# Optimization experiments

Measured on AMD Instinct MI355X. Metric: run time of the kernel, lower is better.

## Reference

```python
import math
import jax, jax.numpy as jnp
import numpy as np

HIDDEN = 1024
NUM_HEADS = 16
HEAD_DIM = HIDDEN // NUM_HEADS
B, S = 4, 2048


def setup_inputs() -> dict:
    key = jax.random.key(0)
    ks = jax.random.split(key, 10)
    sc_in = 1.0 / math.sqrt(HIDDEN)
    inp = {
        "query": jax.random.normal(ks[0], (B, S, HIDDEN), jnp.float32),
        "key": jax.random.normal(ks[1], (B, S, HIDDEN), jnp.float32),
        "value": jax.random.normal(ks[2], (B, S, HIDDEN), jnp.float32),
        "mask": jax.random.randint(ks[3], (B, S), 0, 2).astype(bool),
        # NOTE: ModuleList([Linear]*num_heads) shares ONE Linear across all heads.
        "Wq": jax.random.normal(ks[4], (HIDDEN, HEAD_DIM), jnp.float32) * sc_in,
        "bq": jnp.zeros((HEAD_DIM,), jnp.float32),
        "Wk": jax.random.normal(ks[5], (HIDDEN, HEAD_DIM), jnp.float32) * sc_in,
        "bk": jnp.zeros((HEAD_DIM,), jnp.float32),
        "Wv": jax.random.normal(ks[6], (HIDDEN, HEAD_DIM), jnp.float32) * sc_in,
        "bv": jnp.zeros((HEAD_DIM,), jnp.float32),
        "Wout": jax.random.normal(ks[7], (HIDDEN, HIDDEN), jnp.float32) * sc_in,
        "bout": jnp.zeros((HIDDEN,), jnp.float32),
        "seq_mask": 0,
    }
    return inp


def _layer_norm_scores(x, eps=1e-8):
    # torch.std is unbiased (ddof=1); is_train=False => no affine
    mean = jnp.mean(x, axis=-1, keepdims=True)
    sigma = jnp.std(x, axis=-1, keepdims=True, ddof=1)
    return (x - mean) / (sigma + eps)


def reference(query, key, value, mask, Wq, bq, Wk, bk, Wv, bv, Wout, bout, seq_mask):
    # All heads share identical weights -> compute one head, tile the concat.
    q = query @ Wq + bq          # [B,S,hd]
    k = key @ Wk + bk            # [B,S,hd]
    v = value @ Wv + bv          # [B,S,hd]
    scores = jnp.einsum("bqd,bkd->bqk", q, k) / math.sqrt(HIDDEN)  # [B,S,S]
    scores = _layer_norm_scores(scores)
    m = jnp.broadcast_to(mask[:, None, :], scores.shape)  # [B,S,S]
    if seq_mask:
        tri = jnp.triu(jnp.ones(scores.shape[-2:], bool), k=1)
        m = m | tri[None]
    # original fills with -1e-32 (effectively a no-op bug) -- reproduce exactly
    scores = scores + jnp.where(m, jnp.float32(-1e-32), jnp.float32(0.0))
    attn = jax.nn.softmax(scores, axis=-1)
    head = jnp.einsum("bqk,bkd->bqd", attn, v)   # [B,S,hd]
    attention = jnp.tile(head, (1, 1, NUM_HEADS))  # concat of identical heads
    return attention @ Wout + bout
```

## Files before the change

### kernel.cpp

```cpp
#include <hip/hip_runtime.h>
#include <math.h>

#define B_  4
#define S_  2048
#define H_  1024
#define D_  64
#define ROWS (B_*S_)
#define KSPLIT 8
#define LOG2E 1.4426950408889634f

typedef __attribute__((ext_vector_type(4))) float  floatx4;
typedef __attribute__((ext_vector_type(8))) short  short8;
typedef __attribute__((ext_vector_type(8))) __bf16 bf16x8;

#define WS_KSUM 0
#define WS_M    (WS_KSUM + B_*D_)
#define WS_A2   (WS_M + B_*D_*D_)
#define WS_C2   (WS_A2 + ROWS)
#define WS_SWP  (WS_C2 + ROWS)
#define WS_FEND (WS_SWP + KSPLIT*ROWS)
#define WB_QB  0
#define WB_KF  (WB_QB + ROWS*D_)
#define WB_VF  (WB_KF + ROWS*D_)
#define WB_WT  (WB_VF + ROWS*D_)
#define WB_WFF (WB_WT + 3*D_*H_)
#define WB_OP  (WB_WFF + H_*D_)
#define NZ2    (B_*D_ + B_*D_*D_)

__device__ __forceinline__ unsigned short f2bf(float f) {
    union { float f; unsigned u; } v; v.f = f;
    unsigned r = v.u + 0x7FFFu + ((v.u >> 16) & 1u);
    return (unsigned short)(r >> 16);
}
__device__ __forceinline__ short bfc(float f) {
    __bf16 h = (__bf16)f;
    short s; __builtin_memcpy(&s, &h, 2); return s;
}
__device__ __forceinline__ float bf2f(short s) {
    union { unsigned u; float f; } v;
    v.u = ((unsigned)(unsigned short)s) << 16; return v.f;
}
__device__ __forceinline__ bf16x8 ldb(const short* p) {
    union { short8 s; bf16x8 b; } u; u.s = *(const short8*)p; return u.b;
}
#define MFMA(a,b,c) __builtin_amdgcn_mfma_f32_16x16x32_bf16(a, b, c, 0, 0, 0)
__device__ __forceinline__ void lds_fence() {
    __builtin_amdgcn_wave_barrier();
    __builtin_amdgcn_s_waitcnt(0xc07f);
    __builtin_amdgcn_wave_barrier();
}

__global__ __launch_bounds__(256) void prep(
    const float* __restrict__ Wq, const float* __restrict__ Wk,
    const float* __restrict__ Wv, const float* __restrict__ Wout,
    float* __restrict__ wsf)
{
    __shared__ float tile[64][65];
    short* wsb = (short*)(wsf + WS_FEND);
    const int bx = blockIdx.x, t = threadIdx.x;
    if (bx < 96) {
        int idx = bx * 256 + t;
        int mat = idx >> 13, rem = idx & 8191;
        int kc = rem >> 8, nt = (rem >> 6) & 3, lane = rem & 63;
        int g = lane >> 4, l15 = lane & 15;
        const float* W = (mat == 0) ? Wq : (mat == 1) ? Wk : Wv;
        short8 fr;
        #pragma unroll
        for (int j = 0; j < 8; ++j)
            fr[j] = (short)f2bf(W[(size_t)(kc*32 + g*8 + j) * D_ + nt*16 + l15]);
        *(short8*)&wsb[WB_WT + (size_t)idx * 8] = fr;
    } else if (bx < 112) {
        int n0 = (bx - 96) * 64;
        int nn = t & 63, dg = t >> 6;
        for (int dd = 0; dd < 16; ++dd) {
            int d = dg * 16 + dd;
            float s = 0.0f;
            #pragma unroll
            for (int h = 0; h < 16; ++h)
                s += Wout[(size_t)(h * 64 + d) * H_ + n0 + nn];
            tile[d][nn] = s;
        }
        __syncthreads();
        #pragma unroll
        for (int u = 0; u < 2; ++u) {
            int s = 2*t + u;
            int ctl = s >> 7, h = (s >> 6) & 1, lane = s & 63;
            int g = lane >> 4, l2 = lane & 15;
            short8 fr;
            #pragma unroll
            for (int j = 0; j < 8; ++j)
                fr[j] = (short)f2bf(tile[h*32 + g*8 + j][ctl*16 + l2]);
            *(short8*)&wsb[WB_WFF + (size_t)((((n0 >> 4) + ctl)*2 + h)*64 + lane) * 8] = fr;
        }
    } else {
        int i = (bx - 112) * 256 + t;
        if (i < NZ2) wsf[WS_KSUM + i] = 0.0f;
    }
}

__global__ __launch_bounds__(256) void qkv_mfma(
    const float* __restrict__ query, const float* __restrict__ key,
    const float* __restrict__ value,
    const float* __restrict__ bq, const float* __restrict__ bk,
    const float* __restrict__ bvp, float* __restrict__ wsf)
{
    short* wsb = (short*)(wsf + WS_FEND);
    const int mat = blockIdx.y;
    const float* X    = (mat == 0) ? query : (mat == 1) ? key : value;
    const float* bias = (mat == 0) ? bq    : (mat == 1) ? bk  : bvp;
    const short* WT3 = wsb + WB_WT + (size_t)mat * (D_ * H_);

    const int t = threadIdx.x, w = t >> 6, lane = t & 63;
    const int l15 = lane & 15, g = lane >> 4;
    const int r0 = blockIdx.x * 32;
    const int mrow0 = (w >> 1) * 16;
    const int nt0 = (w & 1) * 2;

    __shared__ short xs[32][136];
    floatx4 acc[2] = {};

    for (int step = 0; step < 8; ++step) {
        __syncthreads();
        #pragma unroll
        for (int u = 0; u < 4; ++u) {
            int row = u * 8 + (t >> 5), col = (t & 31) * 4;
            float4 xv = *(const float4*)&X[(size_t)(r0 + row) * H_ + step * 128 + col];
            short4 pk;
            pk.x = bfc(xv.x); pk.y = bfc(xv.y); pk.z = bfc(xv.z); pk.w = bfc(xv.w);
            *(short4*)&xs[row][col] = pk;
        }
        __syncthreads();
        #pragma unroll
        for (int kk = 0; kk < 4; ++kk) {
            bf16x8 a = ldb(&xs[mrow0 + l15][kk * 32 + g * 8]);
            int kc = step * 4 + kk;
            #pragma unroll
            for (int n = 0; n < 2; ++n) {
                bf16x8 bf = ldb(&WT3[(size_t)((kc * 4) + nt0 + n) * 512 + lane * 8]);
                acc[n] = MFMA(a, bf, acc[n]);
            }
        }
    }

    if (mat == 0) {
        short* QB = wsb + WB_QB;
        #pragma unroll
        for (int n = 0; n < 2; ++n) {
            int col = (nt0 + n) * 16 + l15;
            float bb = bias[col];
            #pragma unroll
            for (int r = 0; r < 4; ++r)
                QB[(size_t)(r0 + mrow0 + 4*g + r) * D_ + col] = (short)f2bf(acc[n][r] + bb);
        }
    } else if (mat == 1) {
        short* KF = wsb + WB_KF;
        #pragma unroll
        for (int n = 0; n < 2; ++n) {
            int d = (nt0 + n) * 16 + l15;
            int kh = d >> 5, gk = (d >> 3) & 3, j = d & 7;
            float bb = bias[d];
            #pragma unroll
            for (int r = 0; r < 4; ++r) {
                int R = r0 + mrow0 + 4*g + r;
                KF[(size_t)(((R >> 4) * 2 + kh) * 64 + gk * 16 + (R & 15)) * 8 + j] =
                    (short)f2bf(acc[n][r] + bb);
            }
        }
    } else {
        short* VF = wsb + WB_VF;
        int R0 = r0 + mrow0 + 4*g;
        int kh = (R0 >> 5) & 1, gv = (R0 >> 3) & 3, j0 = R0 & 7, blk = R0 >> 6;
        #pragma unroll
        for (int n = 0; n < 2; ++n) {
            int d = (nt0 + n) * 16 + l15;
            int ntv = d >> 4;
            float bb = bias[d];
            short4 pk;
            pk.x = (short)f2bf(acc[n][0] + bb); pk.y = (short)f2bf(acc[n][1] + bb);
            pk.z = (short)f2bf(acc[n][2] + bb); pk.w = (short)f2bf(acc[n][3] + bb);
            *(short4*)&VF[(size_t)(((blk * 4 + ntv) * 2 + kh) * 64 + gv * 16 + (d & 15)) * 8 + j0] = pk;
        }
    }
}

__global__ __launch_bounds__(256) void kstats(float* __restrict__ wsf) {
    const short* KF = (short*)(wsf + WS_FEND) + WB_KF;
    const int b     = blockIdx.x >> 5;
    const int chunk = blockIdx.x & 31;
    const int keyblk0 = b * 128 + chunk * 4;

    __shared__ float kt[64][64];
    const int t = threadIdx.x;
    #pragma unroll
    for (int u = 0; u < 2; ++u) {
        int s = 2*t + u;
        int kb4 = s >> 7, kh = (s >> 6) & 1, lane2 = s & 63;
        int g2 = lane2 >> 4, l2 = lane2 & 15;
        short8 v = *(const short8*)&KF[(size_t)(((keyblk0 + kb4) * 2 + kh) * 64 + lane2) * 8];
        #pragma unroll
        for (int j = 0; j < 8; ++j)
            kt[kb4 * 16 + l2][kh * 32 + g2 * 8 + j] = bf2f(v[j]);
    }
    __syncthreads();

    const int td = t >> 4, te = t & 15;
    float acc[4][4] = {};
    for (int j = 0; j < 64; ++j) {
        float4 a  = *(const float4*)&kt[j][td*4];
        float4 bb = *(const float4*)&kt[j][te*4];
        float av[4] = {a.x, a.y, a.z, a.w};
        float bw[4] = {bb.x, bb.y, bb.z, bb.w};
        #pragma unroll
        for (int i = 0; i < 4; ++i)
            #pragma unroll
            for (int l = 0; l < 4; ++l)
                acc[i][l] += av[i] * bw[l];
    }
    float* M = wsf + WS_M + (size_t)b * D_ * D_;
    #pragma unroll
    for (int i = 0; i < 4; ++i)
        #pragma unroll
        for (int l = 0; l < 4; ++l)
            atomicAdd(&M[(td*4 + i) * D_ + te*4 + l], acc[i][l]);

    if (t < 64) {
        float s = 0.0f;
        for (int j = 0; j < 64; ++j) s += kt[j][t];
        atomicAdd(&wsf[WS_KSUM + b * D_ + t], s);
    }
}

__global__ __launch_bounds__(256) void rowstats(float* __restrict__ wsf) {
    const short* Qb = (short*)(wsf + WS_FEND) + WB_QB;
    const int t = threadIdx.x, w = t >> 6, lane = t & 63;
    const int q0 = blockIdx.x * 32 + w * 8;
    const int b  = q0 >> 11;
    const float* M = wsf + WS_M + (size_t)b * D_ * D_;

    float qv[8], y[8] = {};
    #pragma unroll
    for (int r = 0; r < 8; ++r) qv[r] = bf2f(Qb[(size_t)(q0 + r) * D_ + lane]);
    for (int d2 = 0; d2 < 64; ++d2) {
        float m = M[d2 * D_ + lane];
        #pragma unroll
        for (int r = 0; r < 8; ++r) y[r] += __shfl(qv[r], d2, 64) * m;
    }
    float kl = wsf[WS_KSUM + b * D_ + lane];
    float z[8], sv[8];
    #pragma unroll
    for (int r = 0; r < 8; ++r) { z[r] = y[r] * qv[r]; sv[r] = qv[r] * kl; }
    #pragma unroll
    for (int m = 1; m < 64; m <<= 1) {
        #pragma unroll
        for (int r = 0; r < 8; ++r) {
            z[r]  += __shfl_xor(z[r],  m, 64);
            sv[r] += __shfl_xor(sv[r], m, 64);
        }
    }
    #pragma unroll
    for (int r = 0; r < 8; ++r) {
        if (lane == r) {
            float sum   = sv[r] * (1.0f / 32.0f);
            float sumsq = z[r]  * (1.0f / 1024.0f);
            float mu  = sum * (1.0f / 2048.0f);
            float var = (sumsq - sum * sum * (1.0f / 2048.0f)) * (1.0f / 2047.0f);
            var = fmaxf(var, 0.0f);
            float inv = 1.0f / (sqrtf(var) + 1e-8f);
            wsf[WS_A2 + q0 + r] = inv * (LOG2E / 32.0f);
            wsf[WS_C2 + q0 + r] = -mu * inv * LOG2E;
        }
    }
}

__global__ __launch_bounds__(256) void attention(float* __restrict__ wsf) {
    short* wsb = (short*)(wsf + WS_FEND);
    const short* Qb = wsb + WB_QB;
    const short* KF = wsb + WB_KF;
    const short* VF = wsb + WB_VF;
    __shared__ short P[4][32][72];
    __shared__ short stage[2][8192];

    const int t = threadIdx.x, w = t >> 6, lane = t & 63;
    const int l15 = lane & 15, g = lane >> 4;
    const int q0 = blockIdx.x * 128 + w * 32;
    const int b  = blockIdx.x >> 4;
    const int kb = blockIdx.y * (S_ / KSPLIT);

    bf16x8 bqf[2][2];
    float a2v[2], c2v[2];
    #pragma unroll
    for (int nt = 0; nt < 2; ++nt) {
        int q = q0 + nt*16 + l15;
        #pragma unroll
        for (int h = 0; h < 2; ++h)
            bqf[nt][h] = ldb(&Qb[(size_t)q * D_ + h*32 + g*8]);
        a2v[nt] = wsf[WS_A2 + q];
        c2v[nt] = wsf[WS_C2 + q];
    }

    floatx4 O[2][4] = {};
    float sacc[2] = {0.0f, 0.0f};
    short* Pw = &P[w][0][0];

    const int tb = t * 8;
    short8 rr[4];
    {
        const short* KFc = KF + (size_t)((b * S_ + kb) >> 4) * 1024;
        const short* VFc = VF + (size_t)((b * S_ + kb) >> 6) * 4096;
        rr[0] = *(const short8*)&KFc[tb];
        rr[1] = *(const short8*)&KFc[tb + 2048];
        rr[2] = *(const short8*)&VFc[tb];
        rr[3] = *(const short8*)&VFc[tb + 2048];
    }

    for (int kc = 0; kc < S_ / KSPLIT; kc += 64) {
        short* buf = &stage[(kc >> 6) & 1][0];
        __syncthreads();
        *(short8*)&buf[tb]        = rr[0];
        *(short8*)&buf[tb + 2048] = rr[1];
        *(short8*)&buf[tb + 4096] = rr[2];
        *(short8*)&buf[tb + 6144] = rr[3];
        if (kc + 64 < S_ / KSPLIT) {
            const int key1 = kb + kc + 64;
            const short* KFc = KF + (size_t)((b * S_ + key1) >> 4) * 1024;
            const short* VFc = VF + (size_t)((b * S_ + key1) >> 6) * 4096;
            rr[0] = *(const short8*)&KFc[tb];
            rr[1] = *(const short8*)&KFc[tb + 2048];
            rr[2] = *(const short8*)&VFc[tb];
            rr[3] = *(const short8*)&VFc[tb + 2048];
        }
        __syncthreads();

        floatx4 Sc[4][2] = {};
        #pragma unroll
        for (int kt = 0; kt < 4; ++kt) {
            bf16x8 ak0 = ldb(&buf[(kt*2 + 0)*512 + lane*8]);
            bf16x8 ak1 = ldb(&buf[(kt*2 + 1)*512 + lane*8]);
            #pragma unroll
            for (int nt = 0; nt < 2; ++nt) {
                Sc[kt][nt] = MFMA(ak0, bqf[nt][0], Sc[kt][nt]);
                Sc[kt][nt] = MFMA(ak1, bqf[nt][1], Sc[kt][nt]);
            }
        }
        lds_fence();
        #pragma unroll
        for (int nt = 0; nt < 2; ++nt) {
            const float aa = a2v[nt], cc = c2v[nt];
            #pragma unroll
            for (int kt = 0; kt < 4; ++kt) {
                float w0 = exp2f(fmaf(Sc[kt][nt][0], aa, cc));
                float w1 = exp2f(fmaf(Sc[kt][nt][1], aa, cc));
                float w2 = exp2f(fmaf(Sc[kt][nt][2], aa, cc));
                float w3 = exp2f(fmaf(Sc[kt][nt][3], aa, cc));
                sacc[nt] += (w0 + w1) + (w2 + w3);
                short4 pk;
                pk.x = bfc(w0); pk.y = bfc(w1); pk.z = bfc(w2); pk.w = bfc(w3);
                *(short4*)&Pw[(nt*16 + l15) * 72 + kt*16 + 4*g] = pk;
            }
        }
        lds_fence();
        bf16x8 ap[2][2];
        #pragma unroll
        for (int mt = 0; mt < 2; ++mt)
            #pragma unroll
            for (int kh = 0; kh < 2; ++kh)
                ap[mt][kh] = ldb(&Pw[(mt*16 + l15) * 72 + kh*32 + g*8]);
        #pragma unroll
        for (int nt = 0; nt < 4; ++nt) {
            #pragma unroll
            for (int kh = 0; kh < 2; ++kh) {
                bf16x8 bv = ldb(&buf[4096 + (nt*2 + kh)*512 + lane*8]);
                #pragma unroll
                for (int mt = 0; mt < 2; ++mt)
                    O[mt][nt] = MFMA(ap[mt][kh], bv, O[mt][nt]);
            }
        }
    }

    #pragma unroll
    for (int nt = 0; nt < 2; ++nt) {
        sacc[nt] += __shfl_xor(sacc[nt], 16, 64);
        sacc[nt] += __shfl_xor(sacc[nt], 32, 64);
    }
    if (lane < 16) {
        wsf[WS_SWP + blockIdx.y * ROWS + q0 + lane]      = sacc[0];
        wsf[WS_SWP + blockIdx.y * ROWS + q0 + 16 + lane] = sacc[1];
    }
    short* OP = wsb + WB_OP + ((size_t)blockIdx.y * ROWS + q0) * D_;
    #pragma unroll
    for (int mt = 0; mt < 2; ++mt)
        #pragma unroll
        for (int nt = 0; nt < 4; ++nt)
            #pragma unroll
            for (int r = 0; r < 4; ++r)
                OP[(size_t)(mt*16 + 4*g + r) * D_ + nt*16 + l15] =
                    (short)f2bf(O[mt][nt][r]);
}

__global__ __launch_bounds__(256) void outmm(
    const float* __restrict__ bout, const float* __restrict__ wsf,
    float* __restrict__ out)
{
    const short* wsb = (const short*)(wsf + WS_FEND);
    const short* OP  = wsb + WB_OP;
    const short* WFF = wsb + WB_WFF;
    __shared__ short hnF[2 * 64 * 8];

    const int t = threadIdx.x;
    const int row0 = blockIdx.x * 16;

    {
        const int r = t >> 4;
        const int c = (t & 15) * 4;
        const int row = row0 + r;
        float sw = 0.0f;
        #pragma unroll
        for (int p = 0; p < KSPLIT; ++p) sw += wsf[WS_SWP + p * ROWS + row];
        float inv = 1.0f / sw;
        float a0 = 0.f, a1 = 0.f, a2 = 0.f, a3 = 0.f;
        #pragma unroll
        for (int p = 0; p < KSPLIT; ++p) {
            short4 o = *(const short4*)&OP[((size_t)p * ROWS + row) * D_ + c];
            a0 += bf2f(o.x); a1 += bf2f(o.y); a2 += bf2f(o.z); a3 += bf2f(o.w);
        }
        short4 hn;
        hn.x = (short)f2bf(a0 * inv); hn.y = (short)f2bf(a1 * inv);
        hn.z = (short)f2bf(a2 * inv); hn.w = (short)f2bf(a3 * inv);
        int kh = c >> 5, gH = (c >> 3) & 3, j0 = c & 7;
        *(short4*)&hnF[(size_t)(kh * 64 + gH * 16 + r) * 8 + j0] = hn;
    }
    __syncthreads();

    const int w = t >> 6, lane = t & 63, l15 = lane & 15, g = lane >> 4;
    bf16x8 ah0 = ldb(&hnF[(size_t)(0 * 64 + lane) * 8]);
    bf16x8 ah1 = ldb(&hnF[(size_t)(1 * 64 + lane) * 8]);
    #pragma unroll
    for (int i = 0; i < 16; ++i) {
        int n16 = w * 16 + i;
        floatx4 acc = {};
        acc = MFMA(ah0, ldb(&WFF[(size_t)(n16 * 2 + 0) * 512 + lane * 8]), acc);
        acc = MFMA(ah1, ldb(&WFF[(size_t)(n16 * 2 + 1) * 512 + lane * 8]), acc);
        int col = n16 * 16 + l15;
        float bb = bout[col];
        #pragma unroll
        for (int r = 0; r < 4; ++r)
            out[(size_t)(row0 + 4*g + r) * H_ + col] = acc[r] + bb;
    }
}

extern "C" void kernel_launch(void* const* d_in, const int* in_sizes, int n_in,
                              void* d_out, int out_size, void* d_ws, size_t ws_size,
                              hipStream_t stream) {
    const float* query = (const float*)d_in[0];
    const float* key   = (const float*)d_in[1];
    const float* value = (const float*)d_in[2];
    const float* Wq   = (const float*)d_in[4];
    const float* bq   = (const float*)d_in[5];
    const float* Wk   = (const float*)d_in[6];
    const float* bk   = (const float*)d_in[7];
    const float* Wv   = (const float*)d_in[8];
    const float* bv   = (const float*)d_in[9];
    const float* Wout = (const float*)d_in[10];
    const float* bout = (const float*)d_in[11];

    float* ws  = (float*)d_ws;
    float* out = (float*)d_out;

    prep<<<177, 256, 0, stream>>>(Wq, Wk, Wv, Wout, ws);
    qkv_mfma<<<dim3(ROWS/32, 3), 256, 0, stream>>>(query, key, value, bq, bk, bv, ws);
    kstats<<<B_ * 32, 256, 0, stream>>>(ws);
    rowstats<<<ROWS/32, 256, 0, stream>>>(ws);
    attention<<<dim3(ROWS/128, KSPLIT), 256, 0, stream>>>(ws);
    outmm<<<ROWS/16, 256, 0, stream>>>(bout, ws, out);
}
```

Measured before the change: 202.1 us.

## Load K/V fragments directly from global in attention, halve block size, double key split

Removes the double-buffered LDS staging of K and V tiles in the attention kernel. Each wave now loads MFMA fragments straight from global memory. Blocks shrink to two waves with a launch-bounds occupancy hint, and the key dimension is split sixteen ways instead of eight to keep the grid large. It also adds s_setprio around the MFMA sections and uses the hardware exp2 intrinsic. In exchange it loses K/V reuse across waves through LDS, raising L2 traffic, and the final reduction over key splits gets more partials.

```diff
diff --git a/kernel.cpp b/kernel.cpp
--- a/kernel.cpp
+++ b/kernel.cpp
@@ -6,7 +6,7 @@
 #define H_  1024
 #define D_  64
 #define ROWS (B_*S_)
-#define KSPLIT 8
+#define KSPLIT 16
 #define LOG2E 1.4426950408889634f
 
 typedef __attribute__((ext_vector_type(4))) float  floatx4;
@@ -272,18 +272,17 @@
     }
 }
 
-__global__ __launch_bounds__(256) void attention(float* __restrict__ wsf) {
+__global__ __launch_bounds__(128, 3) void attention(float* __restrict__ wsf) {
     short* wsb = (short*)(wsf + WS_FEND);
     const short* Qb = wsb + WB_QB;
     const short* KF = wsb + WB_KF;
     const short* VF = wsb + WB_VF;
-    __shared__ short P[4][32][72];
-    __shared__ short stage[2][8192];
+    __shared__ short P[2][32][72];
 
     const int t = threadIdx.x, w = t >> 6, lane = t & 63;
     const int l15 = lane & 15, g = lane >> 4;
-    const int q0 = blockIdx.x * 128 + w * 32;
-    const int b  = blockIdx.x >> 4;
+    const int q0 = blockIdx.x * 64 + w * 32;
+    const int b  = blockIdx.x >> 5;
     const int kb = blockIdx.y * (S_ / KSPLIT);
 
     bf16x8 bqf[2][2];
@@ -302,56 +301,33 @@
     float sacc[2] = {0.0f, 0.0f};
     short* Pw = &P[w][0][0];
 
-    const int tb = t * 8;
-    short8 rr[4];
-    {
-        const short* KFc = KF + (size_t)((b * S_ + kb) >> 4) * 1024;
-        const short* VFc = VF + (size_t)((b * S_ + kb) >> 6) * 4096;
-        rr[0] = *(const short8*)&KFc[tb];
-        rr[1] = *(const short8*)&KFc[tb + 2048];
-        rr[2] = *(const short8*)&VFc[tb];
-        rr[3] = *(const short8*)&VFc[tb + 2048];
-    }
-
     for (int kc = 0; kc < S_ / KSPLIT; kc += 64) {
-        short* buf = &stage[(kc >> 6) & 1][0];
-        __syncthreads();
-        *(short8*)&buf[tb]        = rr[0];
-        *(short8*)&buf[tb + 2048] = rr[1];
-        *(short8*)&buf[tb + 4096] = rr[2];
-        *(short8*)&buf[tb + 6144] = rr[3];
-        if (kc + 64 < S_ / KSPLIT) {
-            const int key1 = kb + kc + 64;
-            const short* KFc = KF + (size_t)((b * S_ + key1) >> 4) * 1024;
-            const short* VFc = VF + (size_t)((b * S_ + key1) >> 6) * 4096;
-            rr[0] = *(const short8*)&KFc[tb];
-            rr[1] = *(const short8*)&KFc[tb + 2048];
-            rr[2] = *(const short8*)&VFc[tb];
-            rr[3] = *(const short8*)&VFc[tb + 2048];
-        }
-        __syncthreads();
-
+        const int key0 = kb + kc;
+        const int kblk16 = (b * S_ + key0) >> 4;
+        const int kblk64 = (b * S_ + key0) >> 6;
         floatx4 Sc[4][2] = {};
+        __builtin_amdgcn_s_setprio(1);
         #pragma unroll
         for (int kt = 0; kt < 4; ++kt) {
-            bf16x8 ak0 = ldb(&buf[(kt*2 + 0)*512 + lane*8]);
-            bf16x8 ak1 = ldb(&buf[(kt*2 + 1)*512 + lane*8]);
+            bf16x8 ak0 = ldb(&KF[(size_t)(((kblk16 + kt) * 2 + 0) * 64 + lane) * 8]);
+            bf16x8 ak1 = ldb(&KF[(size_t)(((kblk16 + kt) * 2 + 1) * 64 + lane) * 8]);
             #pragma unroll
             for (int nt = 0; nt < 2; ++nt) {
                 Sc[kt][nt] = MFMA(ak0, bqf[nt][0], Sc[kt][nt]);
                 Sc[kt][nt] = MFMA(ak1, bqf[nt][1], Sc[kt][nt]);
             }
         }
+        __builtin_amdgcn_s_setprio(0);
         lds_fence();
         #pragma unroll
         for (int nt = 0; nt < 2; ++nt) {
             const float aa = a2v[nt], cc = c2v[nt];
             #pragma unroll
             for (int kt = 0; kt < 4; ++kt) {
-                float w0 = exp2f(fmaf(Sc[kt][nt][0], aa, cc));
-                float w1 = exp2f(fmaf(Sc[kt][nt][1], aa, cc));
-                float w2 = exp2f(fmaf(Sc[kt][nt][2], aa, cc));
-                float w3 = exp2f(fmaf(Sc[kt][nt][3], aa, cc));
+                float w0 = __builtin_amdgcn_exp2f(fmaf(Sc[kt][nt][0], aa, cc));
+                float w1 = __builtin_amdgcn_exp2f(fmaf(Sc[kt][nt][1], aa, cc));
+                float w2 = __builtin_amdgcn_exp2f(fmaf(Sc[kt][nt][2], aa, cc));
+                float w3 = __builtin_amdgcn_exp2f(fmaf(Sc[kt][nt][3], aa, cc));
                 sacc[nt] += (w0 + w1) + (w2 + w3);
                 short4 pk;
                 pk.x = bfc(w0); pk.y = bfc(w1); pk.z = bfc(w2); pk.w = bfc(w3);
@@ -365,16 +341,18 @@
             #pragma unroll
             for (int kh = 0; kh < 2; ++kh)
                 ap[mt][kh] = ldb(&Pw[(mt*16 + l15) * 72 + kh*32 + g*8]);
+        __builtin_amdgcn_s_setprio(1);
         #pragma unroll
         for (int nt = 0; nt < 4; ++nt) {
             #pragma unroll
             for (int kh = 0; kh < 2; ++kh) {
-                bf16x8 bv = ldb(&buf[4096 + (nt*2 + kh)*512 + lane*8]);
+                bf16x8 bv = ldb(&VF[(size_t)(((kblk64 * 4 + nt) * 2 + kh) * 64 + lane) * 8]);
                 #pragma unroll
                 for (int mt = 0; mt < 2; ++mt)
                     O[mt][nt] = MFMA(ap[mt][kh], bv, O[mt][nt]);
             }
         }
+        __builtin_amdgcn_s_setprio(0);
     }
 
     #pragma unroll
@@ -470,6 +448,6 @@
     qkv_mfma<<<dim3(ROWS/32, 3), 256, 0, stream>>>(query, key, value, bq, bk, bv, ws);
     kstats<<<B_ * 32, 256, 0, stream>>>(ws);
     rowstats<<<ROWS/32, 256, 0, stream>>>(ws);
-    attention<<<dim3(ROWS/128, KSPLIT), 256, 0, stream>>>(ws);
+    attention<<<dim3(ROWS/64, KSPLIT), 128, 0, stream>>>(ws);
     outmm<<<ROWS/16, 256, 0, stream>>>(bout, ws, out);
 }
```

Result: no change. 204.0 us (+0.9%).
